# Kernel tuning notes

Hardware: AMD Instinct MI355X
Metric: run time of the kernel (lower is better)

## Reference

```python
import math
import jax, jax.numpy as jnp
import numpy as np

B, T, C, H = 2, 2048, 768, 12
D = C // H
EPS = 1e-5


def setup_inputs() -> dict:
    key = jax.random.key(0)
    ks = jax.random.split(key, 12)
    s = 0.02
    return {
        "x": jax.random.normal(ks[0], (B, T, C), jnp.float32),
        "Wqkv": jax.random.normal(ks[1], (C, 3 * C), jnp.float32) * s,
        "bqkv": jnp.zeros((3 * C,), jnp.float32),
        "Wo": jax.random.normal(ks[2], (C, C), jnp.float32) * s,
        "bo": jnp.zeros((C,), jnp.float32),
        "ln1_g": jnp.ones((C,), jnp.float32),
        "ln1_b": jnp.zeros((C,), jnp.float32),
        "Wf": jax.random.normal(ks[3], (C, 4 * C), jnp.float32) * s,
        "bf": jnp.zeros((4 * C,), jnp.float32),
        "Wp": jax.random.normal(ks[4], (4 * C, C), jnp.float32) * s,
        "bp": jnp.zeros((C,), jnp.float32),
        "ln2_g": jnp.ones((C,), jnp.float32),
        "ln2_b": jnp.zeros((C,), jnp.float32),
    }


def _layernorm(x, g, b):
    mu = jnp.mean(x, axis=-1, keepdims=True)
    var = jnp.mean(jnp.square(x - mu), axis=-1, keepdims=True)
    return (x - mu) * jax.lax.rsqrt(var + EPS) * g + b


def _attention(x, Wqkv, bqkv):
    qkv = x @ Wqkv + bqkv                      # [B,T,3C]
    q, k, v = jnp.split(qkv, 3, axis=-1)
    q = q.reshape(B, T, H, D)
    k = k.reshape(B, T, H, D)
    v = v.reshape(B, T, H, D)
    # scores: [B,H,T,T] -- deliberately materialized as in the source module
    scores = jnp.einsum('bqhd,bkhd->bhqk', q, k) / math.sqrt(D)
    causal = jnp.tril(jnp.ones((T, T), bool))
    scores = jnp.where(causal, scores, -jnp.inf)
    w = jax.nn.softmax(scores, axis=-1)
    out = jnp.einsum('bhqk,bkhd->bqhd', w, v)
    return out.reshape(B, T, C)


def reference(x, Wqkv, bqkv, Wo, bo, ln1_g, ln1_b, Wf, bf, Wp, bp, ln2_g, ln2_b):
    # attention skip + post-LN
    h = x + _attention(x, Wqkv, bqkv) @ Wo + bo
    h = _layernorm(h, ln1_g, ln1_b)
    # GELU (exact, erf-based, matching nn.GELU default) FFN skip + post-LN
    h = h + jax.nn.gelu(h @ Wf + bf, approximate=False) @ Wp + bp
    h = _layernorm(h, ln2_g, ln2_b)
    return h
```

## Files before the change

### kernel.cpp

```cpp
#include <hip/hip_runtime.h>

#define BB 2
#define TT 2048
#define CC 768
#define HH 12
#define DD 64
#define TBT (BB * TT)

typedef __bf16 bfx8 __attribute__((ext_vector_type(8)));
typedef float f32x4 __attribute__((ext_vector_type(4)));
typedef float f32x16 __attribute__((ext_vector_type(16)));

__device__ __forceinline__ unsigned short f2b(float f) {
  unsigned u = __float_as_uint(f);
  return (unsigned short)((u + 0x7FFFu + ((u >> 16) & 1u)) >> 16);
}
__device__ __forceinline__ float b2f(unsigned short u) {
  return __uint_as_float(((unsigned)u) << 16);
}

__device__ __forceinline__ unsigned pack2bf(float lo, float hi) {
  union { __bf16 h[2]; unsigned u; } x;
  x.h[0] = (__bf16)lo; x.h[1] = (__bf16)hi;
  return x.u;
}

__device__ __forceinline__ void gload_lds16(const void* g, void* l) {
  __builtin_amdgcn_global_load_lds((const __attribute__((address_space(1))) void*)g,
                                   (__attribute__((address_space(3))) void*)l, 16, 0, 0);
}

__device__ __forceinline__ float gelu_fast(float v) {
  float t = v * v;
  float s = fmaf(0.10294663f, t, 2.3021582f);
  float e = __builtin_amdgcn_exp2f(-v * s);
  return v * __builtin_amdgcn_rcpf(1.0f + e);
}

__global__ __launch_bounds__(256) void k_prep(const float* __restrict__ x,
                                              unsigned short* __restrict__ xb,
                                              const float* __restrict__ Wqkv,
                                              unsigned short* __restrict__ WqkvT,
                                              const float* __restrict__ Wo,
                                              unsigned short* __restrict__ WoT,
                                              const float* __restrict__ Wf,
                                              unsigned short* __restrict__ WfT,
                                              const float* __restrict__ Wp,
                                              unsigned short* __restrict__ WpT) {
  __shared__ float tile[32][33];
  int bid = blockIdx.x;
  const int tid = threadIdx.x;
  if (bid < 3072) {
    int i = bid * 1024 + tid * 4;
    float4 v = *(const float4*)(x + i);
    ushort4 o;
    o.x = f2b(v.x); o.y = f2b(v.y); o.z = f2b(v.z); o.w = f2b(v.w);
    *(ushort4*)(xb + i) = o;
    return;
  }
  bid -= 3072;
  const float* W; unsigned short* WT; int K, N, bx, by;
  if (bid < 1728)              { W = Wqkv; WT = WqkvT; K = 768;  N = 2304; bx = bid % 72; by = bid / 72; }
  else if (bid < 1728 + 576)   { bid -= 1728; W = Wo; WT = WoT; K = 768;  N = 768;  bx = bid % 24; by = bid / 24; }
  else if (bid < 1728 + 576 + 2304) { bid -= 1728 + 576; W = Wf; WT = WfT; K = 768; N = 3072; bx = bid % 96; by = bid / 96; }
  else                         { bid -= 1728 + 576 + 2304; W = Wp; WT = WpT; K = 3072; N = 768; bx = bid % 24; by = bid / 24; }
  int n0 = bx * 32, k0 = by * 32;
  int j = tid & 31, i0 = tid >> 5;
  for (int i = i0; i < 32; i += 8) tile[i][j] = W[(size_t)(k0 + i) * N + n0 + j];
  __syncthreads();
  for (int i = i0; i < 32; i += 8) WT[(size_t)(n0 + i) * K + k0 + j] = f2b(tile[j][i]);
}

template<int MODE>
__global__ __launch_bounds__(256) void k_gemm_bt(const unsigned short* __restrict__ A,
                                                 const unsigned short* __restrict__ Bt,
                                                 const float* __restrict__ bias,
                                                 unsigned short* __restrict__ outb,
                                                 unsigned short* __restrict__ vt,
                                                 int M, int N, int K) {
  __shared__ __align__(16) unsigned short SMEM[4][128 * 64];
  const int tid = threadIdx.x;
  const int l = tid & 63, w = tid >> 6;
  const int wr = w >> 1, wc = w & 1;
  const int lr = l & 15, g = l >> 4;

  const int gx = gridDim.x, nwg = gx * gridDim.y;
  const int orig = blockIdx.x + gx * blockIdx.y;
  const int q8 = nwg >> 3;
  const int swz = (orig & 7) * q8 + (orig >> 3);
  const int m0 = (swz / gx) * 128, n0 = (swz % gx) * 128;

  int kbeg = 0, kend = K;
  if (MODE == 3) { int K2 = K >> 1; kbeg = blockIdx.z * K2; kend = kbeg + K2; }

  f32x4 acc[4][4] = {};

  auto stage = [&](int kt, int buf) {
#pragma unroll
    for (int i = 0; i < 4; ++i) {
      int s = tid + i * 256;
      int row = s >> 3;
      int q = (s & 7) ^ (row & 7);
      gload_lds16(A + (size_t)(m0 + row) * K + kt + q * 8, &SMEM[buf][s * 8]);
      gload_lds16(Bt + (size_t)(n0 + row) * K + kt + q * 8, &SMEM[2 + buf][s * 8]);
    }
  };

  stage(kbeg, 0);
  __syncthreads();

  int cur = 0;
  for (int kt = kbeg; kt < kend; kt += 64) {
    if (kt + 64 < kend) stage(kt + 64, cur ^ 1);
    const unsigned short* As = &SMEM[cur][0];
    const unsigned short* Bs = &SMEM[2 + cur][0];
#pragma unroll
    for (int kk = 0; kk < 2; ++kk) {
      bfx8 af[4], bfr[4];
#pragma unroll
      for (int m = 0; m < 4; ++m) {
        int row = wr * 64 + m * 16 + lr;
        int quad = (kk * 4 + g) ^ (row & 7);
        af[m] = *(const bfx8*)(&As[row * 64 + quad * 8]);
      }
#pragma unroll
      for (int n = 0; n < 4; ++n) {
        int row = wc * 64 + n * 16 + lr;
        int quad = (kk * 4 + g) ^ (row & 7);
        bfr[n] = *(const bfx8*)(&Bs[row * 64 + quad * 8]);
      }
#pragma unroll
      for (int m = 0; m < 4; ++m)
#pragma unroll
        for (int n = 0; n < 4; ++n)
          acc[m][n] = __builtin_amdgcn_mfma_f32_16x16x32_bf16(af[m], bfr[n], acc[m][n], 0, 0, 0);
    }
    __syncthreads();
    cur ^= 1;
  }

  if (MODE == 0 && n0 >= 2 * CC) {
    unsigned short* T = &SMEM[0][0];
#pragma unroll
    for (int m = 0; m < 4; ++m)
#pragma unroll
      for (int n = 0; n < 4; ++n) {
        int tcol = wc * 64 + n * 16 + lr;
        float bv = bias[n0 + tcol];
#pragma unroll
        for (int r = 0; r < 4; ++r) {
          int trow = wr * 64 + m * 16 + g * 4 + r;
          T[tcol * 128 + (trow ^ ((tcol & 15) << 3))] = f2b(acc[m][n][r] + bv);
        }
      }
    __syncthreads();
    int tcol = tid >> 1, half = tid & 1;
    int gcol = n0 - 2 * CC + tcol;
    int hh = gcol >> 6, dd = gcol & 63;
    int bloc = m0 >> 11;
    int tb = m0 & 2047;
    unsigned short* dstrow = vt + ((size_t)(bloc * HH + hh) * DD + dd) * TT + tb;
#pragma unroll
    for (int c = 0; c < 8; ++c) {
      int tbase = half * 64 + c * 8;
      bfx8 val = *(const bfx8*)(&T[tcol * 128 + (tbase ^ ((tcol & 15) << 3))]);
      *(bfx8*)(dstrow + tbase) = val;
    }
    return;
  }

  unsigned short* dstb = (MODE == 3) ? (blockIdx.z ? vt : outb) : outb;
#pragma unroll
  for (int m = 0; m < 4; ++m) {
#pragma unroll
    for (int n = 0; n < 4; ++n) {
      int col = n0 + wc * 64 + n * 16 + lr;
      float bv = (MODE == 3) ? 0.f : bias[col];
#pragma unroll
      for (int r = 0; r < 4; ++r) {
        int row = m0 + wr * 64 + m * 16 + g * 4 + r;
        float v = acc[m][n][r] + bv;
        if (MODE == 1) v = gelu_fast(v);
        dstb[(size_t)row * N + col] = f2b(v);
      }
    }
  }
}

#define MFIX 8.0f
__global__ __launch_bounds__(256) void k_attn(const unsigned short* __restrict__ qkv,
                                              const unsigned short* __restrict__ VT,
                                              unsigned short* __restrict__ aout,
                                              unsigned short* __restrict__ opart,
                                              float* __restrict__ lbuf) {
  __shared__ __align__(16) unsigned short Ks[2][2][64 * 64];
  __shared__ __align__(16) unsigned short Vs[2][2][64 * 64];
  const int tid = threadIdx.x;
  const int l = tid & 63, w = tid >> 6;
  const int ql = l & 31, hi = l >> 5;

  const int id = blockIdx.x;
  const int c8 = id & 7;
  const int r8 = id >> 3;
  const int cid = r8 % 40;
  const int bh = (r8 / 40) * 8 + c8;
  const int b = bh / HH, h = bh % HH;

  int bx, sub;
  if (cid < 4)       { bx = cid;                  sub = 0; }
  else if (cid < 12) { bx = 4 + ((cid - 4) >> 1); sub = (cid - 4) & 1; }
  else if (cid < 24) { bx = 8 + (cid - 12) / 3;   sub = (cid - 12) % 3; }
  else               { bx = 12 + ((cid - 24) >> 2); sub = (cid - 24) & 3; }
  const int nt = 2 * bx + 2;
  const int nchunks = (nt + 7) >> 3;
  const int t0i = sub * 8;
  const int tcount = min(8, nt - t0i);
  const int nIter = tcount >> 1;

  const int qw = bx * 128 + w * 32;
  const int qrow = qw + ql;

  const unsigned short* Kbase = qkv + (size_t)(b * TT) * (3 * CC) + CC + h * DD;
  const unsigned short* Vbase = VT + (size_t)bh * DD * TT;

  bfx8 qf[4];
  {
    const unsigned short* qp = qkv + (size_t)(b * TT + qrow) * (3 * CC) + h * DD;
    const float SC = 0.125f * 1.44269504088896340736f;
#pragma unroll
    for (int c = 0; c < 4; ++c) {
      bfx8 rw = *(const bfx8*)(qp + c * 16 + hi * 8);
#pragma unroll
      for (int j = 0; j < 8; ++j) qf[c][j] = (__bf16)((float)rw[j] * SC);
    }
  }

  f32x16 o0 = {}, o1 = {};
  float l_run = 0.f;

  auto stage = [&](int it, int bufi) {
    const int t64 = t0i + it * 2;
#pragma unroll
    for (int half = 0; half < 2; ++half) {
      const int k0 = (t64 + half) * 64;
#pragma unroll
      for (int i = 0; i < 2; ++i) {
        int sl = tid + i * 256;
        int row = sl >> 3;
        int q = (sl & 7) ^ (row & 7);
        gload_lds16(Kbase + (size_t)(k0 + row) * (3 * CC) + q * 8, &Ks[bufi][half][sl * 8]);
        gload_lds16(Vbase + (size_t)row * TT + k0 + q * 8, &Vs[bufi][half][sl * 8]);
      }
    }
  };

  stage(0, 0);
  __syncthreads();

  int cur = 0;
  for (int it = 0; it < nIter; ++it) {
    if (it + 1 < nIter) stage(it + 1, cur ^ 1);

#pragma unroll
    for (int h2 = 0; h2 < 2; ++h2) {
      const int t = t0i + it * 2 + h2;
      const int k0 = t * 64;
      if (k0 <= qw + 31) {
        f32x16 sa[2];
        __builtin_amdgcn_s_setprio(1);
#pragma unroll
        for (int kh = 0; kh < 2; ++kh) {
          f32x16 acc = {};
          int row = kh * 32 + ql;
          int rx = row & 7;
#pragma unroll
          for (int c = 0; c < 4; ++c) {
            int quad = (c * 2 + hi) ^ rx;
            bfx8 kf = *(const bfx8*)(&Ks[cur][h2][row * 64 + quad * 8]);
            acc = __builtin_amdgcn_mfma_f32_32x32x16_bf16(kf, qf[c], acc, 0, 0, 0);
          }
          sa[kh] = acc;
        }
        __builtin_amdgcn_s_setprio(0);

        if (k0 + 63 > qw) {
#pragma unroll
          for (int kh = 0; kh < 2; ++kh)
#pragma unroll
            for (int r = 0; r < 16; ++r) {
              int kk = k0 + kh * 32 + (r & 3) + 8 * (r >> 2) + 4 * hi;
              if (kk > qrow) sa[kh][r] = -1e30f;
            }
        }

        float rs0 = 0.f, rs1 = 0.f, rs2 = 0.f, rs3 = 0.f;
        unsigned pk[2][8];
#pragma unroll
        for (int kh = 0; kh < 2; ++kh)
#pragma unroll
          for (int i = 0; i < 8; ++i) {
            float p0 = __builtin_amdgcn_exp2f(sa[kh][2 * i] - MFIX);
            float p1 = __builtin_amdgcn_exp2f(sa[kh][2 * i + 1] - MFIX);
            float ps = p0 + p1;
            if ((i & 3) == 0) rs0 += ps;
            else if ((i & 3) == 1) rs1 += ps;
            else if ((i & 3) == 2) rs2 += ps;
            else rs3 += ps;
            pk[kh][i] = pack2bf(p0, p1);
          }
        float rs = (rs0 + rs1) + (rs2 + rs3);
        rs += __shfl_xor(rs, 32);
        l_run += rs;

        bfx8 pf[4];
#pragma unroll
        for (int kh = 0; kh < 2; ++kh)
#pragma unroll
          for (int c = 0; c < 2; ++c) {
            unsigned a0 = pk[kh][c * 4 + 0], a1 = pk[kh][c * 4 + 1];
            unsigned b0 = pk[kh][c * 4 + 2], b1 = pk[kh][c * 4 + 3];
            asm volatile("v_permlane32_swap_b32 %0, %1" : "+v"(a0), "+v"(b0));
            asm volatile("v_permlane32_swap_b32 %0, %1" : "+v"(a1), "+v"(b1));
            union { unsigned u[4]; bfx8 v; } cvt;
            cvt.u[0] = a0; cvt.u[1] = a1; cvt.u[2] = b0; cvt.u[3] = b1;
            pf[kh * 2 + c] = cvt.v;
          }

        __builtin_amdgcn_s_setprio(1);
#pragma unroll
        for (int kc = 0; kc < 4; ++kc) {
          {
            int row = ql;
            bfx8 vf = *(const bfx8*)(&Vs[cur][h2][row * 64 + (((kc * 2 + hi) ^ (row & 7)) * 8)]);
            o0 = __builtin_amdgcn_mfma_f32_32x32x16_bf16(vf, pf[kc], o0, 0, 0, 0);
          }
          {
            int row = 32 + ql;
            bfx8 vf = *(const bfx8*)(&Vs[cur][h2][row * 64 + (((kc * 2 + hi) ^ (row & 7)) * 8)]);
            o1 = __builtin_amdgcn_mfma_f32_32x32x16_bf16(vf, pf[kc], o1, 0, 0, 0);
          }
        }
        __builtin_amdgcn_s_setprio(0);
      }
    }

    __syncthreads();
    cur ^= 1;
  }

  if (nchunks == 1) {
    float inv = 1.0f / l_run;
    unsigned short* orow = aout + (size_t)(b * TT + qrow) * CC + h * DD;
#pragma unroll
    for (int dh = 0; dh < 2; ++dh) {
      const f32x16& oo = dh ? o1 : o0;
#pragma unroll
      for (int qd = 0; qd < 4; ++qd) {
        ushort4 v;
        v.x = f2b(oo[qd * 4 + 0] * inv);
        v.y = f2b(oo[qd * 4 + 1] * inv);
        v.z = f2b(oo[qd * 4 + 2] * inv);
        v.w = f2b(oo[qd * 4 + 3] * inv);
        *(ushort4*)(orow + dh * 32 + 8 * qd + 4 * hi) = v;
      }
    }
  } else {
    unsigned short* orow = opart + (size_t)sub * TBT * CC + (size_t)(b * TT + qrow) * CC + h * DD;
#pragma unroll
    for (int dh = 0; dh < 2; ++dh) {
      const f32x16& oo = dh ? o1 : o0;
#pragma unroll
      for (int qd = 0; qd < 4; ++qd) {
        ushort4 v;
        v.x = f2b(oo[qd * 4 + 0]);
        v.y = f2b(oo[qd * 4 + 1]);
        v.z = f2b(oo[qd * 4 + 2]);
        v.w = f2b(oo[qd * 4 + 3]);
        *(ushort4*)(orow + dh * 32 + 8 * qd + 4 * hi) = v;
      }
    }
    if (hi == 0) lbuf[((size_t)sub * (BB * HH) + bh) * TT + qrow] = l_run;
  }
}

__global__ __launch_bounds__(256) void k_attn_combine(const unsigned short* __restrict__ opart,
                                                      const float* __restrict__ lbuf,
                                                      unsigned short* __restrict__ aout) {
  int idx = (blockIdx.x * 256 + threadIdx.x) * 4;
  int bt = idx / CC, c = idx % CC;
  int b = bt >> 11, t = bt & (TT - 1);
  int bx = t >> 7;
  int cnt = (2 * bx + 9) >> 3;
  if (cnt < 2) return;
  int h = c >> 6;
  int bh = b * HH + h;

  float lsum = 0.f;
#pragma unroll
  for (int s = 0; s < 4; ++s)
    if (s < cnt) lsum += lbuf[((size_t)s * (BB * HH) + bh) * TT + t];
  float linv = 1.0f / lsum;

  float a0 = 0.f, a1 = 0.f, a2 = 0.f, a3 = 0.f;
#pragma unroll
  for (int s = 0; s < 4; ++s)
    if (s < cnt) {
      ushort4 v = *(const ushort4*)(opart + (size_t)s * TBT * CC + idx);
      a0 += b2f(v.x);
      a1 += b2f(v.y);
      a2 += b2f(v.z);
      a3 += b2f(v.w);
    }
  ushort4 o;
  o.x = f2b(a0 * linv);
  o.y = f2b(a1 * linv);
  o.z = f2b(a2 * linv);
  o.w = f2b(a3 * linv);
  *(ushort4*)(aout + idx) = o;
}

template<int OUTF32, int RESB16>
__global__ __launch_bounds__(256) void k_layernorm_c(const unsigned short* __restrict__ in0,
                                                     const unsigned short* __restrict__ in1,
                                                     const float* __restrict__ residf,
                                                     const unsigned short* __restrict__ residb,
                                                     const float* __restrict__ biasv,
                                                     const float* __restrict__ gw,
                                                     const float* __restrict__ bw,
                                                     float* __restrict__ outf,
                                                     unsigned short* __restrict__ outb) {
  __shared__ float red[8];
  const int row = blockIdx.x;
  const int tid = threadIdx.x;
  float v[3];
  float s = 0.f;
#pragma unroll
  for (int j = 0; j < 3; ++j) {
    int c = tid + j * 256;
    size_t idx = (size_t)row * CC + c;
    float rv = RESB16 ? b2f(residb[idx]) : residf[idx];
    v[j] = b2f(in0[idx]) + b2f(in1[idx]) + rv + biasv[c];
    s += v[j];
  }
#pragma unroll
  for (int off = 32; off; off >>= 1) s += __shfl_xor(s, off);
  if ((tid & 63) == 0) red[tid >> 6] = s;
  __syncthreads();
  s = red[0] + red[1] + red[2] + red[3];
  float mu = s * (1.0f / CC);
  float qs = 0.f;
#pragma unroll
  for (int j = 0; j < 3; ++j) { float d = v[j] - mu; qs += d * d; }
#pragma unroll
  for (int off = 32; off; off >>= 1) qs += __shfl_xor(qs, off);
  if ((tid & 63) == 0) red[4 + (tid >> 6)] = qs;
  __syncthreads();
  qs = red[4] + red[5] + red[6] + red[7];
  float rstd = rsqrtf(qs * (1.0f / CC) + 1e-5f);
#pragma unroll
  for (int j = 0; j < 3; ++j) {
    int c = tid + j * 256;
    float y = (v[j] - mu) * rstd * gw[c] + bw[c];
    if (OUTF32) outf[(size_t)row * CC + c] = y;
    else        outb[(size_t)row * CC + c] = f2b(y);
  }
}

extern "C" void kernel_launch(void* const* d_in, const int* in_sizes, int n_in,
                              void* d_out, int out_size, void* d_ws, size_t ws_size,
                              hipStream_t stream) {
  (void)in_sizes; (void)n_in; (void)out_size; (void)ws_size;
  const float* x    = (const float*)d_in[0];
  const float* Wqkv = (const float*)d_in[1];
  const float* bqkv = (const float*)d_in[2];
  const float* Wo   = (const float*)d_in[3];
  const float* bo   = (const float*)d_in[4];
  const float* ln1g = (const float*)d_in[5];
  const float* ln1b = (const float*)d_in[6];
  const float* Wf   = (const float*)d_in[7];
  const float* bf_  = (const float*)d_in[8];
  const float* Wp   = (const float*)d_in[9];
  const float* bp   = (const float*)d_in[10];
  const float* ln2g = (const float*)d_in[11];
  const float* ln2b = (const float*)d_in[12];

  char* ws = (char*)d_ws;
  size_t off = 0;
  auto alloc = [&](size_t bytes) {
    void* p = ws + off;
    off += (bytes + 255) & ~(size_t)255;
    return p;
  };
  unsigned short* xb    = (unsigned short*)alloc((size_t)TBT * CC * 2);
  unsigned short* WqkvT = (unsigned short*)alloc((size_t)3 * CC * CC * 2);
  unsigned short* WoT   = (unsigned short*)alloc((size_t)CC * CC * 2);
  unsigned short* WfT   = (unsigned short*)alloc((size_t)4 * CC * CC * 2);
  unsigned short* WpT   = (unsigned short*)alloc((size_t)4 * CC * CC * 2);
  unsigned short* qkvb  = (unsigned short*)alloc((size_t)TBT * 3 * CC * 2);
  unsigned short* VTb   = (unsigned short*)alloc((size_t)TBT * CC * 2);
  float*          hbuf  = (float*)alloc((size_t)TBT * CC * 4);
  unsigned short* hlnb  = (unsigned short*)alloc((size_t)TBT * CC * 2);
  unsigned short* gbuf  = (unsigned short*)alloc((size_t)TBT * 4 * CC * 2);

  unsigned short* aout  = xb;
  unsigned short* opart = gbuf;
  float*          lvals = (float*)hbuf;
  unsigned short* woP0b = gbuf;
  unsigned short* woP1b = gbuf + (size_t)TBT * CC;
  unsigned short* fpP0b = (unsigned short*)hbuf;
  unsigned short* fpP1b = qkvb;

  k_prep<<<9984, 256, 0, stream>>>(x, xb, Wqkv, WqkvT, Wo, WoT, Wf, WfT, Wp, WpT);

  k_gemm_bt<0><<<dim3(3 * CC / 128, TBT / 128), 256, 0, stream>>>(
      xb, WqkvT, bqkv, qkvb, VTb, TBT, 3 * CC, CC);
  k_attn<<<960, 256, 0, stream>>>(qkvb, VTb, aout, opart, lvals);
  k_attn_combine<<<(TBT * CC) / 1024, 256, 0, stream>>>(opart, lvals, aout);
  k_gemm_bt<3><<<dim3(CC / 128, TBT / 128, 2), 256, 0, stream>>>(
      aout, WoT, nullptr, woP0b, woP1b, TBT, CC, CC);
  k_layernorm_c<0, 0><<<TBT, 256, 0, stream>>>(woP0b, woP1b, x, nullptr, bo,
                                               ln1g, ln1b, nullptr, hlnb);
  k_gemm_bt<1><<<dim3(4 * CC / 128, TBT / 128), 256, 0, stream>>>(
      hlnb, WfT, bf_, gbuf, nullptr, TBT, 4 * CC, CC);
  k_gemm_bt<3><<<dim3(CC / 128, TBT / 128, 2), 256, 0, stream>>>(
      gbuf, WpT, nullptr, fpP0b, fpP1b, TBT, CC, 4 * CC);
  k_layernorm_c<1, 1><<<TBT, 256, 0, stream>>>(fpP0b, fpP1b, nullptr, hlnb, bp,
                                               ln2g, ln2b, (float*)d_out, nullptr);
}
```

Measured before the change: 169.3 us.

## Widen attention blocks to 512 threads covering 256 query rows, shrink combine grid

```diff
diff --git a/kernel.cpp b/kernel.cpp
--- a/kernel.cpp
+++ b/kernel.cpp
@@ -188,7 +188,9 @@
 }
 
 #define MFIX 8.0f
-__global__ __launch_bounds__(256) void k_attn(const unsigned short* __restrict__ qkv,
+__device__ const unsigned char CBX8[20]  = {0,1, 2,2, 3,3, 4,4,4, 5,5,5, 6,6,6,6, 7,7,7,7};
+__device__ const unsigned char CSUB8[20] = {0,0, 0,1, 0,1, 0,1,2, 0,1,2, 0,1,2,3, 0,1,2,3};
+__global__ __launch_bounds__(512) void k_attn(const unsigned short* __restrict__ qkv,
                                               const unsigned short* __restrict__ VT,
                                               unsigned short* __restrict__ aout,
                                               unsigned short* __restrict__ opart,
@@ -202,22 +204,19 @@
   const int id = blockIdx.x;
   const int c8 = id & 7;
   const int r8 = id >> 3;
-  const int cid = r8 % 40;
-  const int bh = (r8 / 40) * 8 + c8;
+  const int cid = r8 % 20;
+  const int bh = (r8 / 20) * 8 + c8;
   const int b = bh / HH, h = bh % HH;
 
-  int bx, sub;
-  if (cid < 4)       { bx = cid;                  sub = 0; }
-  else if (cid < 12) { bx = 4 + ((cid - 4) >> 1); sub = (cid - 4) & 1; }
-  else if (cid < 24) { bx = 8 + (cid - 12) / 3;   sub = (cid - 12) % 3; }
-  else               { bx = 12 + ((cid - 24) >> 2); sub = (cid - 24) & 3; }
-  const int nt = 2 * bx + 2;
+  const int bx = CBX8[cid];
+  const int sub = CSUB8[cid];
+  const int nt = 4 * bx + 4;
   const int nchunks = (nt + 7) >> 3;
   const int t0i = sub * 8;
   const int tcount = min(8, nt - t0i);
   const int nIter = tcount >> 1;
 
-  const int qw = bx * 128 + w * 32;
+  const int qw = bx * 256 + w * 32;
   const int qrow = qw + ql;
 
   const unsigned short* Kbase = qkv + (size_t)(b * TT) * (3 * CC) + CC + h * DD;
@@ -243,14 +242,10 @@
 #pragma unroll
     for (int half = 0; half < 2; ++half) {
       const int k0 = (t64 + half) * 64;
-#pragma unroll
-      for (int i = 0; i < 2; ++i) {
-        int sl = tid + i * 256;
-        int row = sl >> 3;
-        int q = (sl & 7) ^ (row & 7);
-        gload_lds16(Kbase + (size_t)(k0 + row) * (3 * CC) + q * 8, &Ks[bufi][half][sl * 8]);
-        gload_lds16(Vbase + (size_t)row * TT + k0 + q * 8, &Vs[bufi][half][sl * 8]);
-      }
+      int row = tid >> 3;
+      int q = (tid & 7) ^ (row & 7);
+      gload_lds16(Kbase + (size_t)(k0 + row) * (3 * CC) + q * 8, &Ks[bufi][half][tid * 8]);
+      gload_lds16(Vbase + (size_t)row * TT + k0 + q * 8, &Vs[bufi][half][tid * 8]);
     }
   };
 
@@ -308,9 +303,7 @@
             else rs3 += ps;
             pk[kh][i] = pack2bf(p0, p1);
           }
-        float rs = (rs0 + rs1) + (rs2 + rs3);
-        rs += __shfl_xor(rs, 32);
-        l_run += rs;
+        l_run += (rs0 + rs1) + (rs2 + rs3);
 
         bfx8 pf[4];
 #pragma unroll
@@ -348,6 +341,8 @@
     cur ^= 1;
   }
 
+  l_run += __shfl_xor(l_run, 32);
+
   if (nchunks == 1) {
     float inv = 1.0f / l_run;
     unsigned short* orow = aout + (size_t)(b * TT + qrow) * CC + h * DD;
@@ -386,12 +381,14 @@
 __global__ __launch_bounds__(256) void k_attn_combine(const unsigned short* __restrict__ opart,
                                                       const float* __restrict__ lbuf,
                                                       unsigned short* __restrict__ aout) {
-  int idx = (blockIdx.x * 256 + threadIdx.x) * 4;
-  int bt = idx / CC, c = idx % CC;
-  int b = bt >> 11, t = bt & (TT - 1);
-  int bx = t >> 7;
-  int cnt = (2 * bx + 9) >> 3;
-  if (cnt < 2) return;
+  int lin = (blockIdx.x * 256 + threadIdx.x) * 4;
+  int b = lin / (1536 * CC);
+  int rem = lin - b * (1536 * CC);
+  int t = 512 + rem / CC;
+  int c = rem % CC;
+  int idx = (b * TT + t) * CC + c;
+  int bx8 = t >> 8;
+  int cnt = (4 * bx8 + 11) >> 3;
   int h = c >> 6;
   int bh = b * HH + h;
 
@@ -514,8 +511,8 @@
 
   k_gemm_bt<0><<<dim3(3 * CC / 128, TBT / 128), 256, 0, stream>>>(
       xb, WqkvT, bqkv, qkvb, VTb, TBT, 3 * CC, CC);
-  k_attn<<<960, 256, 0, stream>>>(qkvb, VTb, aout, opart, lvals);
-  k_attn_combine<<<(TBT * CC) / 1024, 256, 0, stream>>>(opart, lvals, aout);
+  k_attn<<<480, 512, 0, stream>>>(qkvb, VTb, aout, opart, lvals);
+  k_attn_combine<<<(BB * 1536 * CC) / 1024, 256, 0, stream>>>(opart, lvals, aout);
   k_gemm_bt<3><<<dim3(CC / 128, TBT / 128, 2), 256, 0, stream>>>(
       aout, WoT, nullptr, woP0b, woP1b, TBT, CC, CC);
   k_layernorm_c<0, 0><<<TBT, 256, 0, stream>>>(woP0b, woP1b, x, nullptr, bo,
```

Measured after the change: 163.9 us. -3.2%, faster.
